# Optimization experiments

Measured on AMD Instinct MI355X. Metric: run time of the kernel, lower is better.

The kernel has to match this reference:

```python
import jax, jax.numpy as jnp
import numpy as np

B = 64          # graphs per batch
NP = 512        # nodes per graph (equal-sized graphs)
N = B * NP      # total nodes
E = 1_048_576   # total edges (avg degree 32)
F_IN, H, K, OUT = 16, 128, 2, 2
BN_EPS = 1e-5
EPS = 1e-15


def setup_inputs() -> dict:
    key = jax.random.key(0)
    ks = jax.random.split(key, 12)
    node_feature = jax.random.normal(ks[0], (N, F_IN), jnp.float32)
    # edges constrained to stay within each graph of NP nodes
    g = jax.random.randint(ks[1], (E,), 0, B)
    src = g * NP + jax.random.randint(ks[2], (E,), 0, NP)
    dst = g * NP + jax.random.randint(ks[3], (E,), 0, NP)
    edge_index = jnp.stack([src, dst]).astype(jnp.int32)
    edge_feature = jax.random.uniform(ks[4], (E, 1), jnp.float32)
    batch = (jnp.arange(N, dtype=jnp.int32) // NP)

    def lin(k, i, o):
        return (jax.random.normal(k, (i, o), jnp.float32) / np.sqrt(i)).astype(jnp.float32)

    params = dict(
        W_pre=lin(ks[5], F_IN, H), b_pre=jnp.zeros((H,), jnp.float32),
        W1_rel=lin(ks[6], H, H), b1_rel=jnp.zeros((H,), jnp.float32), W1_root=lin(ks[7], H, H),
        g1=jnp.ones((H,), jnp.float32), be1=jnp.zeros((H,), jnp.float32),
        W2_rel=lin(ks[8], H, H), b2_rel=jnp.zeros((H,), jnp.float32), W2_root=lin(ks[9], H, H),
        g2=jnp.ones((H,), jnp.float32), be2=jnp.zeros((H,), jnp.float32),
        W_pool=lin(ks[10], H, K), b_pool=jnp.zeros((K,), jnp.float32),
        W_post=lin(ks[11], 2 * H, OUT), b_post=jnp.zeros((OUT,), jnp.float32),
    )
    return dict(node_feature=node_feature, edge_index=edge_index,
                edge_feature=edge_feature, batch=batch, **params)


def _graph_conv(x, src, dst, ew, W_rel, b_rel, W_root):
    # PyG GraphConv: out = lin_rel(sum_{j->i} w_e * x_j) + lin_root(x_i)
    msg = x[src] * ew                       # [E, H] gather + scale
    agg = jnp.zeros_like(x).at[dst].add(msg)  # scatter-add to targets
    return agg @ W_rel + b_rel + x @ W_root


def _bn(x, g, b):
    # BatchNorm1d in training mode: batch statistics over nodes (biased var)
    mu = x.mean(0)
    var = jnp.mean((x - mu) ** 2, axis=0)
    return (x - mu) * jax.lax.rsqrt(var + BN_EPS) * g + b


def reference(node_feature, edge_index, edge_feature, batch,
              W_pre, b_pre, W1_rel, b1_rel, W1_root, g1, be1,
              W2_rel, b2_rel, W2_root, g2, be2,
              W_pool, b_pool, W_post, b_post):
    src, dst = edge_index[0], edge_index[1]
    x = node_feature @ W_pre + b_pre
    x = jax.nn.relu(_bn(_graph_conv(x, src, dst, edge_feature, W1_rel, b1_rel, W1_root), g1, be1))
    x = jax.nn.relu(_bn(_graph_conv(x, src, dst, edge_feature, W2_rel, b2_rel, W2_root), g2, be2))
    # dropout p=0.0 -> identity

    # to_dense_batch: equal-sized sorted graphs -> reshape; mask is all-ones
    xd = x.reshape(B, NP, H)
    # to_dense_adj: scatter edge weights into [B, NP, NP]
    gid, ls, ld = src // NP, src % NP, dst % NP
    adj = jnp.zeros((B, NP, NP), jnp.float32).at[gid, ls, ld].add(edge_feature[:, 0])

    # dense_mincut_pool
    s = jax.nn.softmax(xd @ W_pool + b_pool, axis=-1)          # [B, NP, K]
    out = jnp.einsum('bnk,bnh->bkh', s, xd)                     # [B, K, H]
    out_adj = jnp.einsum('bnk,bnm,bml->bkl', s, adj, s)         # [B, K, K]

    mincut_num = jnp.trace(out_adj, axis1=1, axis2=2)
    d_flat = adj.sum(-1)                                        # [B, NP]
    den_mat = jnp.einsum('bnk,bn,bnl->bkl', s, d_flat, s)
    mincut_den = jnp.trace(den_mat, axis1=1, axis2=2)
    mc_loss = jnp.mean(-(mincut_num / mincut_den))

    ss = jnp.einsum('bnk,bnl->bkl', s, s)                       # [B, K, K]
    ss_n = jnp.linalg.norm(ss, axis=(-2, -1), keepdims=True)
    i_s = jnp.eye(K, dtype=ss.dtype)
    o_loss = jnp.mean(jnp.linalg.norm(ss / ss_n - i_s / jnp.sqrt(jnp.float32(K)), axis=(-2, -1)))

    h = jax.nn.relu(out).reshape(B, K * H)
    logits = h @ W_post + b_post
    return (logits, mc_loss, o_loss)
```

## Files before the change

kernel.cpp:

```cpp
#include <hip/hip_runtime.h>

#define NN 32768
#define NP 512
#define NB 64
#define NE 1048576
#define FIN 16
#define H 128
#define BN_EPS 1e-5f
#define EPB 4096
#define NBLK (NE / EPB)
#define CAPH 8704
#define NSH 16

typedef unsigned int u32;
typedef unsigned short u16;
typedef __attribute__((ext_vector_type(8))) short bf16x8;
typedef __attribute__((ext_vector_type(4))) float f32x4;

__device__ __forceinline__ u16 f2bf(float f) {
    u32 u = __float_as_uint(f);
    return (u16)((u + 0x7fffu + ((u >> 16) & 1u)) >> 16);
}
__device__ __forceinline__ float bfLo(u32 p) { return __uint_as_float(p << 16); }
__device__ __forceinline__ float bfHi(u32 p) { return __uint_as_float(p & 0xffff0000u); }
__device__ __forceinline__ float b2f(u16 v) { return __uint_as_float((u32)v << 16); }

static constexpr size_t SZ_HALF   = (size_t)NN * H * 2;
static constexpr size_t OFF_X     = 0;
static constexpr size_t OFF_AGG   = OFF_X + SZ_HALF;
static constexpr size_t OFF_TMP   = OFF_AGG;
static constexpr size_t OFF_SORT  = OFF_AGG + SZ_HALF;
static constexpr size_t OFF_OFFS  = OFF_SORT + (size_t)NE * 8;
static constexpr size_t OFF_HISTG = OFF_OFFS + ((size_t)NN + 128) * 4;
static constexpr size_t OFF_STARTG= OFF_HISTG + (size_t)NBLK * NB * 4;
static constexpr size_t OFF_GBASE = OFF_STARTG + (size_t)NBLK * NB * 4;
static constexpr size_t OFF_WT1   = OFF_GBASE + 512;
static constexpr size_t OFF_WT2   = OFF_WT1 + (size_t)H * 2 * H * 2;
static constexpr size_t OFF_S     = OFF_WT2 + (size_t)H * 2 * H * 2;
static constexpr size_t OFF_GST   = OFF_S + (size_t)NN * 2 * 4;
static constexpr size_t OFF_ZERO  = OFF_GST + 1024;
static constexpr size_t OFF_NUM   = OFF_ZERO;
static constexpr size_t OFF_DEN   = OFF_NUM + 256;
static constexpr size_t OFF_BN    = OFF_DEN + 256;
static constexpr size_t SZ_BNL    = (size_t)NSH * 2 * H * 4;
static constexpr size_t OFF_POOL  = OFF_BN + 2 * SZ_BNL;
static constexpr size_t ZERO_BYTES= (OFF_POOL + (size_t)NB * 2 * H * 4) - OFF_ZERO;


__global__ __launch_bounds__(256) void k_prep(
        const float* __restrict__ nf, const float* __restrict__ Wp,
        const float* __restrict__ bp,
        const float* __restrict__ W1_rel, const float* __restrict__ W1_root,
        const float* __restrict__ W2_rel, const float* __restrict__ W2_root,
        const int* __restrict__ src,
        u16* __restrict__ x0, u16* __restrict__ WT1, u16* __restrict__ WT2,
        int* __restrict__ histG) {
    int t = threadIdx.x, bid = blockIdx.x;
    if (bid < 2048) {
        __shared__ float sW[FIN * H];
        __shared__ float sNF[16 * FIN];
        for (int i = t; i < FIN * H; i += 256) sW[i] = Wp[i];
        int n0 = bid * 16;
        sNF[t] = nf[n0 * FIN + t];
        __syncthreads();
        int col = t & 127, half = t >> 7;
        float b = bp[col];
        #pragma unroll
        for (int r = 0; r < 8; ++r) {
            int rr = half * 8 + r;
            float acc = b;
            #pragma unroll
            for (int f = 0; f < FIN; ++f) acc += sNF[rr * FIN + f] * sW[f * H + col];
            x0[(size_t)(n0 + rr) * H + col] = f2bf(acc);
        }
    } else if (bid < 2304) {
        int base = bid - 2048;
        const float* __restrict__ Wrel = (base < 128) ? W1_rel : W2_rel;
        const float* __restrict__ Wroot = (base < 128) ? W1_root : W2_root;
        u16* WT = (base < 128) ? WT1 : WT2;
        int i = (base & 127) * 256 + t;
        int c = i >> 8, k = i & 255;
        float v = (k < H) ? Wrel[k * H + c] : Wroot[(k - H) * H + c];
        WT[c * 256 + k] = f2bf(v);
    } else {
        __shared__ int h[NB];
        if (t < NB) h[t] = 0;
        __syncthreads();
        int ebase = (bid - 2304) * EPB;
        #pragma unroll
        for (int i = 0; i < EPB / 256; ++i) {
            int s = src[ebase + i * 256 + t];
            atomicAdd(&h[s >> 9], 1);
        }
        __syncthreads();
        if (t < NB) histG[(bid - 2304) * NB + t] = h[t];
    }
}

__global__ __launch_bounds__(1024) void k_scanG(const int* __restrict__ histG,
                                                int* __restrict__ startG,
                                                int* __restrict__ gbase) {
    __shared__ int csum[16][64];
    __shared__ int gpre[64];
    int t = threadIdx.x;
    int g = t & 63, c = t >> 6;
    int vals[16];
    int s = 0;
    #pragma unroll
    for (int i = 0; i < 16; ++i) {
        vals[i] = histG[(c * 16 + i) * NB + g];
        s += vals[i];
    }
    csum[c][g] = s;
    __syncthreads();
    int pre = 0;
    for (int i = 0; i < c; ++i) pre += csum[i][g];
    if (c == 0) {
        int tot = 0;
        #pragma unroll
        for (int i = 0; i < 16; ++i) tot += csum[i][g];
        int x = tot;
        #pragma unroll
        for (int o = 1; o < 64; o <<= 1) {
            int y = __shfl_up(x, o);
            if (g >= o) x += y;
        }
        gpre[g] = x - tot;
        gbase[g] = x - tot;
        if (g == 63) gbase[64] = x;
    }
    __syncthreads();
    int run = gpre[g] + pre;
    #pragma unroll
    for (int i = 0; i < 16; ++i) {
        startG[(c * 16 + i) * NB + g] = run;
        run += vals[i];
    }
}

__global__ __launch_bounds__(256) void k_scatterA(
        const int* __restrict__ src, const int* __restrict__ dst,
        const float* __restrict__ ew, const int* __restrict__ histG,
        const int* __restrict__ startG, int2* __restrict__ tmp) {
    __shared__ int lstart[NB + 1];
    __shared__ int cursor[NB];
    __shared__ int gdst[NB];
    __shared__ int2 buf[EPB];
    int t = threadIdx.x, bid = blockIdx.x;
    if (t < NB) {
        int c = histG[bid * NB + t];
        int x = c;
        #pragma unroll
        for (int o = 1; o < 64; o <<= 1) {
            int y = __shfl_up(x, o);
            if (t >= o) x += y;
        }
        lstart[t] = x - c;
        cursor[t] = x - c;
        gdst[t] = startG[bid * NB + t];
        if (t == 63) lstart[NB] = x;
    }
    __syncthreads();
    int ebase = bid * EPB;
    #pragma unroll
    for (int i = 0; i < EPB / 256; ++i) {
        int e = ebase + i * 256 + t;
        int s = src[e], d = dst[e];
        float w = ew[e];
        int g = s >> 9;
        int meta = (s & 511) | ((d & 511) << 9);
        int p = atomicAdd(&cursor[g], 1);
        buf[p] = make_int2(meta, __float_as_int(w));
    }
    __syncthreads();
    for (int i = t; i < EPB; i += 256) {
        int lo = 0;
        #pragma unroll
        for (int stp = 32; stp; stp >>= 1)
            if (lstart[lo + stp] <= i) lo += stp;
        tmp[gdst[lo] + (i - lstart[lo])] = buf[i];
    }
}

__global__ __launch_bounds__(512) void k_sortB(
        const int2* __restrict__ tmp, const int* __restrict__ gbase,
        int2* __restrict__ sorted, int* __restrict__ offs) {
    __shared__ int hist[NP];
    __shared__ int start[NP + 1];
    __shared__ int cursor[NP / 2];
    __shared__ int wsum[8];
    __shared__ int perm[CAPH];
    int t = threadIdx.x;
    int lane = t & 63, wv = t >> 6;
    int g = blockIdx.x >> 1, half = blockIdx.x & 1;
    int gbeg = gbase[g], gend = gbase[g + 1];
    int cnt = gend - gbeg;
    hist[t] = 0;
    __syncthreads();
    for (int i = t; i < cnt; i += 512) {
        int meta = tmp[gbeg + i].x;
        atomicAdd(&hist[(meta >> 9) & 511], 1);
    }
    __syncthreads();
    int c = hist[t];
    int x = c;
    #pragma unroll
    for (int o = 1; o < 64; o <<= 1) {
        int y = __shfl_up(x, o);
        if (lane >= o) x += y;
    }
    if (lane == 63) wsum[wv] = x;
    __syncthreads();
    int off = 0;
    #pragma unroll
    for (int i = 0; i < 8; ++i) off += (i < wv) ? wsum[i] : 0;
    start[t] = off + x - c;
    if (t == 511) start[NP] = off + x;
    __syncthreads();
    int h0 = half * 256;
    if (t < 256) {
        int n = h0 + t;
        offs[g * NP + n] = gbeg + start[n];
        cursor[t] = start[n];
    }
    if (blockIdx.x == 0 && t == 0) offs[NN] = NE;
    __syncthreads();
    int ha = start[h0];
    int hb = half ? cnt : start[256];
    for (int i = t; i < cnt; i += 512) {
        int meta = tmp[gbeg + i].x;
        int d = (meta >> 9) & 511;
        if ((d >> 8) == half) {
            int p = atomicAdd(&cursor[d - h0], 1);
            perm[p - ha] = i;
        }
    }
    __syncthreads();
    for (int o = ha + t; o < hb; o += 512) {
        sorted[gbeg + o] = tmp[gbeg + perm[o - ha]];
    }
}

__global__ __launch_bounds__(256) void k_agg(const u16* __restrict__ x,
        const int* __restrict__ offs, const int2* __restrict__ rec,
        u16* __restrict__ agg) {
    int wv = threadIdx.x >> 6, lane = threadIdx.x & 63;
    int b = blockIdx.x;
    int swz = (b & 7) * (NN / 8 / 4) + (b >> 3);
    int node = swz * 4 + wv;
    int sbase = node & ~(NP - 1);
    const u16* xg = x + (size_t)sbase * H;
    int beg = offs[node], end = offs[node + 1];
    float a0 = 0.f, a1 = 0.f;
    int j = beg;
    for (; j + 4 <= end; j += 4) {
        int2 r0 = rec[j], r1 = rec[j + 1], r2 = rec[j + 2], r3 = rec[j + 3];
        u32 p0 = *(const u32*)(xg + (size_t)(r0.x & 511) * H + 2 * lane);
        u32 p1 = *(const u32*)(xg + (size_t)(r1.x & 511) * H + 2 * lane);
        u32 p2 = *(const u32*)(xg + (size_t)(r2.x & 511) * H + 2 * lane);
        u32 p3 = *(const u32*)(xg + (size_t)(r3.x & 511) * H + 2 * lane);
        float w0 = __int_as_float(r0.y), w1 = __int_as_float(r1.y);
        float w2 = __int_as_float(r2.y), w3 = __int_as_float(r3.y);
        a0 += w0 * bfLo(p0); a1 += w0 * bfHi(p0);
        a0 += w1 * bfLo(p1); a1 += w1 * bfHi(p1);
        a0 += w2 * bfLo(p2); a1 += w2 * bfHi(p2);
        a0 += w3 * bfLo(p3); a1 += w3 * bfHi(p3);
    }
    for (; j < end; ++j) {
        int2 r = rec[j];
        u32 p = *(const u32*)(xg + (size_t)(r.x & 511) * H + 2 * lane);
        float w = __int_as_float(r.y);
        a0 += w * bfLo(p); a1 += w * bfHi(p);
    }
    u32 packed = (u32)f2bf(a0) | ((u32)f2bf(a1) << 16);
    *(u32*)(agg + (size_t)node * H + 2 * lane) = packed;
}

__global__ __launch_bounds__(256) void k_gemm(
        const u16* __restrict__ Amat, const u16* Xmat,
        const u16* __restrict__ WT, const float* __restrict__ brel,
        u16* Y, float* __restrict__ bn_base) {
    __shared__ u16 sWT[128][264];
    __shared__ float colS[128], colQ[128];
    int tid = threadIdx.x;
    int w = tid >> 6, lane = tid & 63;
    int lr = lane & 15, lg = lane >> 4;
    int row0 = blockIdx.x * 64;
    int myrow = row0 + w * 16 + lr;

    bf16x8 af[8];
    const u16* pa = Amat + (size_t)myrow * H + lg * 8;
    const u16* px = Xmat + (size_t)myrow * H + lg * 8;
    #pragma unroll
    for (int kt = 0; kt < 4; ++kt) af[kt] = *(const bf16x8*)(pa + kt * 32);
    #pragma unroll
    for (int kt = 0; kt < 4; ++kt) af[4 + kt] = *(const bf16x8*)(px + kt * 32);

    for (int i = tid; i < 128 * 32; i += 256) {
        int r = i >> 5, c = i & 31;
        *(uint4*)&sWT[r][c * 8] = *(const uint4*)(WT + r * 256 + c * 8);
    }
    if (tid < 128) { colS[tid] = 0.f; colQ[tid] = 0.f; }
    __syncthreads();

    f32x4 acc[8];
    #pragma unroll
    for (int nt = 0; nt < 8; ++nt) acc[nt] = (f32x4){0.f, 0.f, 0.f, 0.f};

    #pragma unroll
    for (int kt = 0; kt < 8; ++kt) {
        #pragma unroll
        for (int nt = 0; nt < 8; ++nt) {
            bf16x8 bf = *(const bf16x8*)&sWT[nt * 16 + lr][kt * 32 + lg * 8];
            acc[nt] = __builtin_amdgcn_mfma_f32_16x16x32_bf16(af[kt], bf, acc[nt], 0, 0, 0);
        }
    }

    float cs[8], cq[8];
    #pragma unroll
    for (int nt = 0; nt < 8; ++nt) {
        int col = nt * 16 + lr;
        float bias = brel[col];
        float s = 0.f, q = 0.f;
        #pragma unroll
        for (int j = 0; j < 4; ++j) {
            float v = acc[nt][j] + bias;
            int row = row0 + w * 16 + lg * 4 + j;
            Y[(size_t)row * H + col] = f2bf(v);
            s += v; q += v * v;
        }
        cs[nt] = s; cq[nt] = q;
    }
    #pragma unroll
    for (int nt = 0; nt < 8; ++nt) {
        cs[nt] += __shfl_xor(cs[nt], 16); cs[nt] += __shfl_xor(cs[nt], 32);
        cq[nt] += __shfl_xor(cq[nt], 16); cq[nt] += __shfl_xor(cq[nt], 32);
    }
    if (lg == 0) {
        #pragma unroll
        for (int nt = 0; nt < 8; ++nt) {
            atomicAdd(&colS[nt * 16 + lr], cs[nt]);
            atomicAdd(&colQ[nt * 16 + lr], cq[nt]);
        }
    }
    __syncthreads();
    if (tid < 128) {
        int sh = blockIdx.x & (NSH - 1);
        atomicAdd(&bn_base[(sh * 2 + 0) * H + tid], colS[tid]);
        atomicAdd(&bn_base[(sh * 2 + 1) * H + tid], colQ[tid]);
    }
}

__global__ __launch_bounds__(256) void k_bnrelu(u16* __restrict__ y,
        const float* __restrict__ bn_base, const float* __restrict__ g,
        const float* __restrict__ be) {
    __shared__ float scL[H], shL[H];
    int t = threadIdx.x;
    if (t < H) {
        float su = 0.f, sq = 0.f;
        #pragma unroll
        for (int sh = 0; sh < NSH; ++sh) {
            su += bn_base[(sh * 2 + 0) * H + t];
            sq += bn_base[(sh * 2 + 1) * H + t];
        }
        float mu = su * (1.f / NN);
        float var = sq * (1.f / NN) - mu * mu;
        float sc = rsqrtf(var + BN_EPS) * g[t];
        scL[t] = sc;
        shL[t] = be[t] - mu * sc;
    }
    __syncthreads();
    #pragma unroll
    for (int it = 0; it < 4; ++it) {
        int idx = blockIdx.x * 1024 + it * 256 + t;
        int c = (idx & 15) * 8;
        uint4 u = ((const uint4*)y)[idx];
        u32 uu[4] = {u.x, u.y, u.z, u.w};
        u32 ro[4];
        #pragma unroll
        for (int p = 0; p < 4; ++p) {
            float v0 = fmaxf(fmaf(bfLo(uu[p]), scL[c + 2 * p], shL[c + 2 * p]), 0.f);
            float v1 = fmaxf(fmaf(bfHi(uu[p]), scL[c + 2 * p + 1], shL[c + 2 * p + 1]), 0.f);
            ro[p] = (u32)f2bf(v0) | ((u32)f2bf(v1) << 16);
        }
        uint4 o; o.x = ro[0]; o.y = ro[1]; o.z = ro[2]; o.w = ro[3];
        ((uint4*)y)[idx] = o;
    }
}

__global__ __launch_bounds__(256) void k_bnrelu_s(u16* __restrict__ y,
        const float* __restrict__ bn_base, const float* __restrict__ g,
        const float* __restrict__ be, const float* __restrict__ Wp,
        const float* __restrict__ bp, float* __restrict__ s) {
    __shared__ float scL[H], shL[H];
    int t = threadIdx.x;
    if (t < H) {
        float su = 0.f, sq = 0.f;
        #pragma unroll
        for (int sh = 0; sh < NSH; ++sh) {
            su += bn_base[(sh * 2 + 0) * H + t];
            sq += bn_base[(sh * 2 + 1) * H + t];
        }
        float mu = su * (1.f / NN);
        float var = sq * (1.f / NN) - mu * mu;
        float sc = rsqrtf(var + BN_EPS) * g[t];
        scL[t] = sc;
        shL[t] = be[t] - mu * sc;
    }
    __syncthreads();
    #pragma unroll
    for (int it = 0; it < 4; ++it) {
        int idx = blockIdx.x * 1024 + it * 256 + t;
        int c = (idx & 15) * 8;
        uint4 u = ((const uint4*)y)[idx];
        u32 uu[4] = {u.x, u.y, u.z, u.w};
        u32 ro[4];
        float z0 = 0.f, z1 = 0.f;
        #pragma unroll
        for (int p = 0; p < 4; ++p) {
            float v0 = fmaxf(fmaf(bfLo(uu[p]), scL[c + 2 * p], shL[c + 2 * p]), 0.f);
            float v1 = fmaxf(fmaf(bfHi(uu[p]), scL[c + 2 * p + 1], shL[c + 2 * p + 1]), 0.f);
            ro[p] = (u32)f2bf(v0) | ((u32)f2bf(v1) << 16);
            z0 += v0 * Wp[(c + 2 * p) * 2] + v1 * Wp[(c + 2 * p + 1) * 2];
            z1 += v0 * Wp[(c + 2 * p) * 2 + 1] + v1 * Wp[(c + 2 * p + 1) * 2 + 1];
        }
        uint4 o; o.x = ro[0]; o.y = ro[1]; o.z = ro[2]; o.w = ro[3];
        ((uint4*)y)[idx] = o;
        #pragma unroll
        for (int off = 8; off; off >>= 1) {
            z0 += __shfl_down(z0, off);
            z1 += __shfl_down(z1, off);
        }
        if ((t & 15) == 0) {
            int row = idx >> 4;
            z0 += bp[0]; z1 += bp[1];
            float m = fmaxf(z0, z1);
            float e0 = expf(z0 - m), e1 = expf(z1 - m);
            float inv = 1.f / (e0 + e1);
            s[row * 2] = e0 * inv;
            s[row * 2 + 1] = e1 * inv;
        }
    }
}

__global__ __launch_bounds__(256) void k_pool_edge(
        const u16* __restrict__ x, const float* __restrict__ s,
        const int2* __restrict__ sorted, const int* __restrict__ gbase,
        float* __restrict__ pool, float* __restrict__ num,
        float* __restrict__ den, float* __restrict__ gst) {
    int bid = blockIdx.x, t = threadIdx.x;
    if (bid < 256) {
        int b = bid & 63, chunk = bid >> 6;
        int h = t & 127, sub = t >> 7;
        int n0 = b * NP + chunk * 128 + sub * 64;
        float a0 = 0.f, a1 = 0.f;
        for (int i = 0; i < 64; ++i) {
            float2 sv = ((const float2*)s)[n0 + i];
            float xv = b2f(x[(size_t)(n0 + i) * H + h]);
            a0 += sv.x * xv;
            a1 += sv.y * xv;
        }
        atomicAdd(&pool[(b * 2 + 0) * H + h], a0);
        atomicAdd(&pool[(b * 2 + 1) * H + h], a1);
    } else {
        __shared__ float2 sl[NP];
        __shared__ float ln[4], ld2[4];
        int ebid = bid - 256;
        int g = ebid >> 2, q = ebid & 3;
        int gbeg = gbase[g], gend = gbase[g + 1];
        for (int i = t; i < NP; i += 256) sl[i] = ((const float2*)s)[g * NP + i];
        __syncthreads();
        float an = 0.f, ad = 0.f;
        int cnt = gend - gbeg;
        int q0 = gbeg + (cnt * q) / 4, q1 = gbeg + (cnt * (q + 1)) / 4;
        for (int i = q0 + t; i < q1; i += 256) {
            int2 r = sorted[i];
            float w = __int_as_float(r.y);
            float2 ss = sl[r.x & 511];
            float2 sd = sl[(r.x >> 9) & 511];
            an += w * (ss.x * sd.x + ss.y * sd.y);
            ad += w * (ss.x * ss.x + ss.y * ss.y);
        }
        for (int o = 32; o; o >>= 1) { an += __shfl_down(an, o); ad += __shfl_down(ad, o); }
        if ((t & 63) == 0) { ln[t >> 6] = an; ld2[t >> 6] = ad; }
        __syncthreads();
        if (t == 0) {
            atomicAdd(&num[g], ln[0] + ln[1] + ln[2] + ln[3]);
            atomicAdd(&den[g], ld2[0] + ld2[1] + ld2[2] + ld2[3]);
        }
        if (q == 0) {
            float p00 = 0.f, p01 = 0.f, p11 = 0.f;
            for (int i = t; i < NP; i += 256) {
                float2 sv = sl[i];
                p00 += sv.x * sv.x;
                p01 += sv.x * sv.y;
                p11 += sv.y * sv.y;
            }
            for (int o = 32; o; o >>= 1) {
                p00 += __shfl_down(p00, o);
                p01 += __shfl_down(p01, o);
                p11 += __shfl_down(p11, o);
            }
            __shared__ float tp[3][4];
            if ((t & 63) == 0) {
                int w = t >> 6;
                tp[0][w] = p00; tp[1][w] = p01; tp[2][w] = p11;
            }
            __syncthreads();
            if (t == 0) {
                gst[g] = tp[0][0] + tp[0][1] + tp[0][2] + tp[0][3];
                gst[NB + g] = tp[1][0] + tp[1][1] + tp[1][2] + tp[1][3];
                gst[2 * NB + g] = tp[2][0] + tp[2][1] + tp[2][2] + tp[2][3];
            }
        }
    }
}

__global__ void k_logits_losses(const float* __restrict__ pool, const float* __restrict__ Wpost,
                                const float* __restrict__ bpost, const float* __restrict__ num,
                                const float* __restrict__ den, const float* __restrict__ gst,
                                float* __restrict__ out) {
    int t = threadIdx.x;
    if (blockIdx.x < 64) {
        int b = blockIdx.x;
        float v = pool[b * 256 + t];
        v = v > 0.f ? v : 0.f;
        float p0 = v * Wpost[t * 2], p1 = v * Wpost[t * 2 + 1];
        for (int o = 32; o; o >>= 1) { p0 += __shfl_down(p0, o); p1 += __shfl_down(p1, o); }
        __shared__ float t0[4], t1[4];
        if ((t & 63) == 0) { t0[t >> 6] = p0; t1[t >> 6] = p1; }
        __syncthreads();
        if (t == 0) {
            out[b * 2] = t0[0] + t0[1] + t0[2] + t0[3] + bpost[0];
            out[b * 2 + 1] = t1[0] + t1[1] + t1[2] + t1[3] + bpost[1];
        }
    } else if (t < 64) {
        float s00 = gst[t], s01 = gst[NB + t], s11 = gst[2 * NB + t];
        float mc = -(num[t] / den[t]);
        float nrm = sqrtf(s00 * s00 + 2.f * s01 * s01 + s11 * s11);
        const float a = 0.70710678118654752440f;
        float d00 = s00 / nrm - a, d01 = s01 / nrm, d11 = s11 / nrm - a;
        float ol = sqrtf(d00 * d00 + 2.f * d01 * d01 + d11 * d11);
        for (int o = 32; o; o >>= 1) { mc += __shfl_down(mc, o); ol += __shfl_down(ol, o); }
        if (t == 0) {
            out[NB * 2] = mc * (1.f / NB);
            out[NB * 2 + 1] = ol * (1.f / NB);
        }
    }
}

extern "C" void kernel_launch(void* const* d_in, const int* in_sizes, int n_in,
                              void* d_out, int out_size, void* d_ws, size_t ws_size,
                              hipStream_t stream) {
    const float* nf     = (const float*)d_in[0];
    const int*   ei     = (const int*)d_in[1];
    const float* ew     = (const float*)d_in[2];
    const float* W_pre  = (const float*)d_in[4];
    const float* b_pre  = (const float*)d_in[5];
    const float* W1_rel = (const float*)d_in[6];
    const float* b1_rel = (const float*)d_in[7];
    const float* W1_root= (const float*)d_in[8];
    const float* g1     = (const float*)d_in[9];
    const float* be1    = (const float*)d_in[10];
    const float* W2_rel = (const float*)d_in[11];
    const float* b2_rel = (const float*)d_in[12];
    const float* W2_root= (const float*)d_in[13];
    const float* g2     = (const float*)d_in[14];
    const float* be2    = (const float*)d_in[15];
    const float* W_pool = (const float*)d_in[16];
    const float* b_pool = (const float*)d_in[17];
    const float* W_post = (const float*)d_in[18];
    const float* b_post = (const float*)d_in[19];

    char* ws = (char*)d_ws;
    u16*   bufX   = (u16*)(ws + OFF_X);
    u16*   bufAgg = (u16*)(ws + OFF_AGG);
    int2*  tmp    = (int2*)(ws + OFF_TMP);
    int2*  sorted = (int2*)(ws + OFF_SORT);
    int*   offs   = (int*)(ws + OFF_OFFS);
    int*   histG  = (int*)(ws + OFF_HISTG);
    int*   startG = (int*)(ws + OFF_STARTG);
    int*   gbase  = (int*)(ws + OFF_GBASE);
    u16*   WT1    = (u16*)(ws + OFF_WT1);
    u16*   WT2    = (u16*)(ws + OFF_WT2);
    float* sarr   = (float*)(ws + OFF_S);
    float* gst    = (float*)(ws + OFF_GST);
    float* numA   = (float*)(ws + OFF_NUM);
    float* denA   = (float*)(ws + OFF_DEN);
    float* bn     = (float*)(ws + OFF_BN);
    float* pool   = (float*)(ws + OFF_POOL);
    float* outF   = (float*)d_out;

    const int* srcA = ei;
    const int* dstA = ei + NE;
    float* bn1 = bn;
    float* bn2 = (float*)(ws + OFF_BN + SZ_BNL);

    hipMemsetAsync(ws + OFF_ZERO, 0, ZERO_BYTES, stream);

    k_prep<<<2560, 256, 0, stream>>>(nf, W_pre, b_pre, W1_rel, W1_root,
                                     W2_rel, W2_root, srcA, bufX, WT1, WT2, histG);
    k_scanG<<<1, 1024, 0, stream>>>(histG, startG, gbase);
    k_scatterA<<<NBLK, 256, 0, stream>>>(srcA, dstA, ew, histG, startG, tmp);
    k_sortB<<<2 * NB, 512, 0, stream>>>(tmp, gbase, sorted, offs);

    k_agg<<<NN / 4, 256, 0, stream>>>(bufX, offs, sorted, bufAgg);
    k_gemm<<<NN / 64, 256, 0, stream>>>(bufAgg, bufX, WT1, b1_rel, bufX, bn1);
    k_bnrelu<<<512, 256, 0, stream>>>(bufX, bn1, g1, be1);

    k_agg<<<NN / 4, 256, 0, stream>>>(bufX, offs, sorted, bufAgg);
    k_gemm<<<NN / 64, 256, 0, stream>>>(bufAgg, bufX, WT2, b2_rel, bufX, bn2);
    k_bnrelu_s<<<512, 256, 0, stream>>>(bufX, bn2, g2, be2, W_pool, b_pool, sarr);

    k_pool_edge<<<512, 256, 0, stream>>>(bufX, sarr, sorted, gbase, pool, numA, denA, gst);
    k_logits_losses<<<NB + 1, 256, 0, stream>>>(pool, W_post, b_post, numA, denA, gst, outF);
}
```

Measured before the change: 275.8 us.

## Fuse mincut pooling into BN-ReLU-softmax kernel and unroll edge aggregation deeper

The s-weighted pooling sum is now computed inside the second BN/ReLU/softmax kernel. Each thread accumulates s*x for its 8 features, reduces in shared memory, then does one global atomic per graph feature. This removes the separate pooling pass that re-read the activation buffer, and the edge-loss kernel becomes its own smaller launch. The aggregation loop now handles 8 edges per step with two independent accumulator pairs to expose more memory-level parallelism. The BN statistic shard count doubles to reduce atomic contention. Each block still does 256-way float atomics to global pool, and the accumulation order changes.

```diff
diff --git a/kernel.cpp b/kernel.cpp
--- a/kernel.cpp
+++ b/kernel.cpp
@@ -10,7 +10,7 @@
 #define EPB 4096
 #define NBLK (NE / EPB)
 #define CAPH 8704
-#define NSH 16
+#define NSH 32
 
 typedef unsigned int u32;
 typedef unsigned short u16;
@@ -23,7 +23,6 @@
 }
 __device__ __forceinline__ float bfLo(u32 p) { return __uint_as_float(p << 16); }
 __device__ __forceinline__ float bfHi(u32 p) { return __uint_as_float(p & 0xffff0000u); }
-__device__ __forceinline__ float b2f(u16 v) { return __uint_as_float((u32)v << 16); }
 
 static constexpr size_t SZ_HALF   = (size_t)NN * H * 2;
 static constexpr size_t OFF_X     = 0;
@@ -251,27 +250,47 @@
     int sbase = node & ~(NP - 1);
     const u16* xg = x + (size_t)sbase * H;
     int beg = offs[node], end = offs[node + 1];
-    float a0 = 0.f, a1 = 0.f;
+    float a0 = 0.f, a1 = 0.f, b0 = 0.f, b1 = 0.f;
     int j = beg;
-    for (; j + 4 <= end; j += 4) {
+    for (; j + 8 <= end; j += 8) {
         int2 r0 = rec[j], r1 = rec[j + 1], r2 = rec[j + 2], r3 = rec[j + 3];
+        int2 r4 = rec[j + 4], r5 = rec[j + 5], r6 = rec[j + 6], r7 = rec[j + 7];
         u32 p0 = *(const u32*)(xg + (size_t)(r0.x & 511) * H + 2 * lane);
         u32 p1 = *(const u32*)(xg + (size_t)(r1.x & 511) * H + 2 * lane);
         u32 p2 = *(const u32*)(xg + (size_t)(r2.x & 511) * H + 2 * lane);
         u32 p3 = *(const u32*)(xg + (size_t)(r3.x & 511) * H + 2 * lane);
+        u32 p4 = *(const u32*)(xg + (size_t)(r4.x & 511) * H + 2 * lane);
+        u32 p5 = *(const u32*)(xg + (size_t)(r5.x & 511) * H + 2 * lane);
+        u32 p6 = *(const u32*)(xg + (size_t)(r6.x & 511) * H + 2 * lane);
+        u32 p7 = *(const u32*)(xg + (size_t)(r7.x & 511) * H + 2 * lane);
         float w0 = __int_as_float(r0.y), w1 = __int_as_float(r1.y);
         float w2 = __int_as_float(r2.y), w3 = __int_as_float(r3.y);
+        float w4 = __int_as_float(r4.y), w5 = __int_as_float(r5.y);
+        float w6 = __int_as_float(r6.y), w7 = __int_as_float(r7.y);
         a0 += w0 * bfLo(p0); a1 += w0 * bfHi(p0);
-        a0 += w1 * bfLo(p1); a1 += w1 * bfHi(p1);
+        b0 += w1 * bfLo(p1); b1 += w1 * bfHi(p1);
         a0 += w2 * bfLo(p2); a1 += w2 * bfHi(p2);
-        a0 += w3 * bfLo(p3); a1 += w3 * bfHi(p3);
-    }
-    for (; j < end; ++j) {
+        b0 += w3 * bfLo(p3); b1 += w3 * bfHi(p3);
+        a0 += w4 * bfLo(p4); a1 += w4 * bfHi(p4);
+        b0 += w5 * bfLo(p5); b1 += w5 * bfHi(p5);
+        a0 += w6 * bfLo(p6); a1 += w6 * bfHi(p6);
+        b0 += w7 * bfLo(p7); b1 += w7 * bfHi(p7);
+    }
+    for (; j + 2 <= end; j += 2) {
+        int2 r0 = rec[j], r1 = rec[j + 1];
+        u32 p0 = *(const u32*)(xg + (size_t)(r0.x & 511) * H + 2 * lane);
+        u32 p1 = *(const u32*)(xg + (size_t)(r1.x & 511) * H + 2 * lane);
+        float w0 = __int_as_float(r0.y), w1 = __int_as_float(r1.y);
+        a0 += w0 * bfLo(p0); a1 += w0 * bfHi(p0);
+        b0 += w1 * bfLo(p1); b1 += w1 * bfHi(p1);
+    }
+    if (j < end) {
         int2 r = rec[j];
         u32 p = *(const u32*)(xg + (size_t)(r.x & 511) * H + 2 * lane);
         float w = __int_as_float(r.y);
         a0 += w * bfLo(p); a1 += w * bfHi(p);
     }
+    a0 += b0; a1 += b1;
     u32 packed = (u32)f2bf(a0) | ((u32)f2bf(a1) << 16);
     *(u32*)(agg + (size_t)node * H + 2 * lane) = packed;
 }
@@ -391,8 +410,10 @@
 __global__ __launch_bounds__(256) void k_bnrelu_s(u16* __restrict__ y,
         const float* __restrict__ bn_base, const float* __restrict__ g,
         const float* __restrict__ be, const float* __restrict__ Wp,
-        const float* __restrict__ bp, float* __restrict__ s) {
+        const float* __restrict__ bp, float* __restrict__ s,
+        float* __restrict__ pool) {
     __shared__ float scL[H], shL[H];
+    __shared__ float poolL[256];
     int t = threadIdx.x;
     if (t < H) {
         float su = 0.f, sq = 0.f;
@@ -407,111 +428,108 @@
         scL[t] = sc;
         shL[t] = be[t] - mu * sc;
     }
-    __syncthreads();
+    poolL[t] = 0.f;
+    __syncthreads();
+    int graph = blockIdx.x >> 3;
+    int c = (t & 15) * 8;
+    float pa0[8], pa1[8];
+    #pragma unroll
+    for (int j = 0; j < 8; ++j) { pa0[j] = 0.f; pa1[j] = 0.f; }
     #pragma unroll
     for (int it = 0; it < 4; ++it) {
         int idx = blockIdx.x * 1024 + it * 256 + t;
-        int c = (idx & 15) * 8;
         uint4 u = ((const uint4*)y)[idx];
         u32 uu[4] = {u.x, u.y, u.z, u.w};
         u32 ro[4];
-        float z0 = 0.f, z1 = 0.f;
+        float v[8];
         #pragma unroll
         for (int p = 0; p < 4; ++p) {
-            float v0 = fmaxf(fmaf(bfLo(uu[p]), scL[c + 2 * p], shL[c + 2 * p]), 0.f);
-            float v1 = fmaxf(fmaf(bfHi(uu[p]), scL[c + 2 * p + 1], shL[c + 2 * p + 1]), 0.f);
-            ro[p] = (u32)f2bf(v0) | ((u32)f2bf(v1) << 16);
-            z0 += v0 * Wp[(c + 2 * p) * 2] + v1 * Wp[(c + 2 * p + 1) * 2];
-            z1 += v0 * Wp[(c + 2 * p) * 2 + 1] + v1 * Wp[(c + 2 * p + 1) * 2 + 1];
+            v[2 * p] = fmaxf(fmaf(bfLo(uu[p]), scL[c + 2 * p], shL[c + 2 * p]), 0.f);
+            v[2 * p + 1] = fmaxf(fmaf(bfHi(uu[p]), scL[c + 2 * p + 1], shL[c + 2 * p + 1]), 0.f);
+            ro[p] = (u32)f2bf(v[2 * p]) | ((u32)f2bf(v[2 * p + 1]) << 16);
         }
         uint4 o; o.x = ro[0]; o.y = ro[1]; o.z = ro[2]; o.w = ro[3];
         ((uint4*)y)[idx] = o;
-        #pragma unroll
-        for (int off = 8; off; off >>= 1) {
-            z0 += __shfl_down(z0, off);
-            z1 += __shfl_down(z1, off);
-        }
-        if ((t & 15) == 0) {
-            int row = idx >> 4;
-            z0 += bp[0]; z1 += bp[1];
-            float m = fmaxf(z0, z1);
-            float e0 = expf(z0 - m), e1 = expf(z1 - m);
-            float inv = 1.f / (e0 + e1);
-            s[row * 2] = e0 * inv;
-            s[row * 2 + 1] = e1 * inv;
-        }
-    }
-}
-
-__global__ __launch_bounds__(256) void k_pool_edge(
-        const u16* __restrict__ x, const float* __restrict__ s,
+        float z0 = 0.f, z1 = 0.f;
+        #pragma unroll
+        for (int j = 0; j < 8; ++j) {
+            z0 += v[j] * Wp[(c + j) * 2];
+            z1 += v[j] * Wp[(c + j) * 2 + 1];
+        }
+        #pragma unroll
+        for (int o2 = 8; o2; o2 >>= 1) { z0 += __shfl_xor(z0, o2); z1 += __shfl_xor(z1, o2); }
+        z0 += bp[0]; z1 += bp[1];
+        float m = fmaxf(z0, z1);
+        float e0 = expf(z0 - m), e1 = expf(z1 - m);
+        float inv = 1.f / (e0 + e1);
+        float s0 = e0 * inv, s1 = e1 * inv;
+        int row = idx >> 4;
+        if ((t & 15) == 0) { s[row * 2] = s0; s[row * 2 + 1] = s1; }
+        #pragma unroll
+        for (int j = 0; j < 8; ++j) { pa0[j] += s0 * v[j]; pa1[j] += s1 * v[j]; }
+    }
+    #pragma unroll
+    for (int j = 0; j < 8; ++j) {
+        atomicAdd(&poolL[c + j], pa0[j]);
+        atomicAdd(&poolL[128 + c + j], pa1[j]);
+    }
+    __syncthreads();
+    if (t < 128) atomicAdd(&pool[(graph * 2 + 0) * H + t], poolL[t]);
+    else atomicAdd(&pool[(graph * 2 + 1) * H + (t - 128)], poolL[t]);
+}
+
+__global__ __launch_bounds__(256) void k_edge(
         const int2* __restrict__ sorted, const int* __restrict__ gbase,
-        float* __restrict__ pool, float* __restrict__ num,
+        const float* __restrict__ s, float* __restrict__ num,
         float* __restrict__ den, float* __restrict__ gst) {
-    int bid = blockIdx.x, t = threadIdx.x;
-    if (bid < 256) {
-        int b = bid & 63, chunk = bid >> 6;
-        int h = t & 127, sub = t >> 7;
-        int n0 = b * NP + chunk * 128 + sub * 64;
-        float a0 = 0.f, a1 = 0.f;
-        for (int i = 0; i < 64; ++i) {
-            float2 sv = ((const float2*)s)[n0 + i];
-            float xv = b2f(x[(size_t)(n0 + i) * H + h]);
-            a0 += sv.x * xv;
-            a1 += sv.y * xv;
-        }
-        atomicAdd(&pool[(b * 2 + 0) * H + h], a0);
-        atomicAdd(&pool[(b * 2 + 1) * H + h], a1);
-    } else {
-        __shared__ float2 sl[NP];
-        __shared__ float ln[4], ld2[4];
-        int ebid = bid - 256;
-        int g = ebid >> 2, q = ebid & 3;
-        int gbeg = gbase[g], gend = gbase[g + 1];
-        for (int i = t; i < NP; i += 256) sl[i] = ((const float2*)s)[g * NP + i];
-        __syncthreads();
-        float an = 0.f, ad = 0.f;
-        int cnt = gend - gbeg;
-        int q0 = gbeg + (cnt * q) / 4, q1 = gbeg + (cnt * (q + 1)) / 4;
-        for (int i = q0 + t; i < q1; i += 256) {
-            int2 r = sorted[i];
-            float w = __int_as_float(r.y);
-            float2 ss = sl[r.x & 511];
-            float2 sd = sl[(r.x >> 9) & 511];
-            an += w * (ss.x * sd.x + ss.y * sd.y);
-            ad += w * (ss.x * ss.x + ss.y * ss.y);
-        }
-        for (int o = 32; o; o >>= 1) { an += __shfl_down(an, o); ad += __shfl_down(ad, o); }
-        if ((t & 63) == 0) { ln[t >> 6] = an; ld2[t >> 6] = ad; }
+    __shared__ float2 sl[NP];
+    __shared__ float ln[4], ld2[4];
+    int t = threadIdx.x;
+    int g = blockIdx.x >> 2, q = blockIdx.x & 3;
+    int gbeg = gbase[g], gend = gbase[g + 1];
+    for (int i = t; i < NP; i += 256) sl[i] = ((const float2*)s)[g * NP + i];
+    __syncthreads();
+    float an = 0.f, ad = 0.f;
+    int cnt = gend - gbeg;
+    int q0 = gbeg + (cnt * q) / 4, q1 = gbeg + (cnt * (q + 1)) / 4;
+    for (int i = q0 + t; i < q1; i += 256) {
+        int2 r = sorted[i];
+        float w = __int_as_float(r.y);
+        float2 ss = sl[r.x & 511];
+        float2 sd = sl[(r.x >> 9) & 511];
+        an += w * (ss.x * sd.x + ss.y * sd.y);
+        ad += w * (ss.x * ss.x + ss.y * ss.y);
+    }
+    for (int o = 32; o; o >>= 1) { an += __shfl_down(an, o); ad += __shfl_down(ad, o); }
+    if ((t & 63) == 0) { ln[t >> 6] = an; ld2[t >> 6] = ad; }
+    __syncthreads();
+    if (t == 0) {
+        atomicAdd(&num[g], ln[0] + ln[1] + ln[2] + ln[3]);
+        atomicAdd(&den[g], ld2[0] + ld2[1] + ld2[2] + ld2[3]);
+    }
+    if (q == 0) {
+        float p00 = 0.f, p01 = 0.f, p11 = 0.f;
+        for (int i = t; i < NP; i += 256) {
+            float2 sv = sl[i];
+            p00 += sv.x * sv.x;
+            p01 += sv.x * sv.y;
+            p11 += sv.y * sv.y;
+        }
+        for (int o = 32; o; o >>= 1) {
+            p00 += __shfl_down(p00, o);
+            p01 += __shfl_down(p01, o);
+            p11 += __shfl_down(p11, o);
+        }
+        __shared__ float tp[3][4];
+        if ((t & 63) == 0) {
+            int w = t >> 6;
+            tp[0][w] = p00; tp[1][w] = p01; tp[2][w] = p11;
+        }
         __syncthreads();
         if (t == 0) {
-            atomicAdd(&num[g], ln[0] + ln[1] + ln[2] + ln[3]);
-            atomicAdd(&den[g], ld2[0] + ld2[1] + ld2[2] + ld2[3]);
-        }
-        if (q == 0) {
-            float p00 = 0.f, p01 = 0.f, p11 = 0.f;
-            for (int i = t; i < NP; i += 256) {
-                float2 sv = sl[i];
-                p00 += sv.x * sv.x;
-                p01 += sv.x * sv.y;
-                p11 += sv.y * sv.y;
-            }
-            for (int o = 32; o; o >>= 1) {
-                p00 += __shfl_down(p00, o);
-                p01 += __shfl_down(p01, o);
-                p11 += __shfl_down(p11, o);
-            }
-            __shared__ float tp[3][4];
-            if ((t & 63) == 0) {
-                int w = t >> 6;
-                tp[0][w] = p00; tp[1][w] = p01; tp[2][w] = p11;
-            }
-            __syncthreads();
-            if (t == 0) {
-                gst[g] = tp[0][0] + tp[0][1] + tp[0][2] + tp[0][3];
-                gst[NB + g] = tp[1][0] + tp[1][1] + tp[1][2] + tp[1][3];
-                gst[2 * NB + g] = tp[2][0] + tp[2][1] + tp[2][2] + tp[2][3];
-            }
+            gst[g] = tp[0][0] + tp[0][1] + tp[0][2] + tp[0][3];
+            gst[NB + g] = tp[1][0] + tp[1][1] + tp[1][2] + tp[1][3];
+            gst[2 * NB + g] = tp[2][0] + tp[2][1] + tp[2][2] + tp[2][3];
         }
     }
 }
@@ -610,8 +628,8 @@
 
     k_agg<<<NN / 4, 256, 0, stream>>>(bufX, offs, sorted, bufAgg);
     k_gemm<<<NN / 64, 256, 0, stream>>>(bufAgg, bufX, WT2, b2_rel, bufX, bn2);
-    k_bnrelu_s<<<512, 256, 0, stream>>>(bufX, bn2, g2, be2, W_pool, b_pool, sarr);
-
-    k_pool_edge<<<512, 256, 0, stream>>>(bufX, sarr, sorted, gbase, pool, numA, denA, gst);
+    k_bnrelu_s<<<512, 256, 0, stream>>>(bufX, bn2, g2, be2, W_pool, b_pool, sarr, pool);
+
+    k_edge<<<256, 256, 0, stream>>>(sorted, gbase, sarr, numA, denA, gst);
     k_logits_losses<<<NB + 1, 256, 0, stream>>>(pool, W_post, b_post, numA, denA, gst, outF);
 }
```

New measurement: 280.0 us. About the same (+1.5%).
